# Kernel tuning notes

Hardware: AMD Instinct MI355X
Metric: run time of the kernel (lower is better)

## Reference

```python
import jax, jax.numpy as jnp
import numpy as np

EPS = 1e-5
D_MODEL, D_STATE, D_CONV, D_INNER, NHEADS, HEADDIM = 256, 64, 4, 512, 8, 64
CONV_DIM = D_INNER + 2 * D_STATE          # 640
D_IN_PROJ = 2 * D_INNER + 2 * D_STATE + NHEADS  # 1160


def _conv_bn_relu(h, w, b, g, beta, m, v, stride, pad):
    # Conv2d + eval-mode BatchNorm2d + ReLU (dropout = identity in eval)
    y = jax.lax.conv_general_dilated(h, w, stride, pad,
                                     dimension_numbers=("NCHW", "OIHW", "NCHW"))
    y = y + b[None, :, None, None]
    scale = (g / jnp.sqrt(v + EPS))[None, :, None, None]
    y = (y - m[None, :, None, None]) * scale + beta[None, :, None, None]
    return jax.nn.relu(y)


def _forward(x, c1w, c1b, bn1g, bn1b, bn1m, bn1v,
             c2w, c2b, bn2g, bn2b, bn2m, bn2v,
             c3w, c3b, bn3g, bn3b, bn3m, bn3v,
             mw_in, mconv_w, mconv_b, mdt_bias, mA_log, mD, mnorm_w, mw_out,
             f1w, f1b, bn4g, bn4b, bn4m, bn4v, f2w, f2b):
    Bsz = x.shape[0]
    h = x[:, None, :, :]                                        # (B,1,H,W)
    h = _conv_bn_relu(h, c1w, c1b, bn1g, bn1b, bn1m, bn1v, (1, 4), [(0, 0), (25, 25)])
    h = jax.lax.reduce_window(h, -jnp.inf, jax.lax.max,
                              (1, 1, 1, 4), (1, 1, 1, 4), "VALID")  # MaxPool (1,4)
    h = _conv_bn_relu(h, c2w, c2b, bn2g, bn2b, bn2m, bn2v, (1, 2), [(0, 0), (10, 10)])
    h = _conv_bn_relu(h, c3w, c3b, bn3g, bn3b, bn3m, bn3v, (1, 2), [(0, 0), (4, 4)])
    h = jnp.mean(h, axis=(2, 3))                                # AdaptiveAvgPool2d((1,1)) -> (B,256)
    xs = h[:, None, :]                                          # (B, L=1, d_model)
    L = xs.shape[1]

    # ---- Mamba2 block ----
    zxbcdt = xs @ mw_in.T                                       # (B,L,1160)
    z = zxbcdt[..., :D_INNER]
    xBC = zxbcdt[..., D_INNER:D_INNER + CONV_DIM]
    dt = zxbcdt[..., -NHEADS:]

    # causal depthwise conv1d + silu
    xc = jnp.transpose(xBC, (0, 2, 1))                          # (B,conv_dim,L)
    xc = jnp.pad(xc, ((0, 0), (0, 0), (D_CONV - 1, 0)))
    xc = jax.lax.conv_general_dilated(xc, mconv_w, (1,), [(0, 0)],
                                      feature_group_count=CONV_DIM,
                                      dimension_numbers=("NCH", "OIH", "NCH"))
    xc = xc + mconv_b[None, :, None]
    xBC = jax.nn.silu(jnp.transpose(xc, (0, 2, 1)))

    xin = xBC[..., :D_INNER]
    Bm = xBC[..., D_INNER:D_INNER + D_STATE]                    # (B,L,d_state), ngroups=1
    Cm = xBC[..., -D_STATE:]

    dt = jax.nn.softplus(dt + mdt_bias)                         # (B,L,nh)
    A = -jnp.exp(mA_log)                                        # (nh,)
    xh = xin.reshape(Bsz, L, NHEADS, HEADDIM)
    dA = jnp.exp(dt * A)                                        # (B,L,nh)
    dtx = dt[..., None] * xh                                    # (B,L,nh,hd)

    def step(hstate, t):
        dA_t, dtx_t, B_t, C_t = t
        hstate = dA_t[:, :, None, None] * hstate + dtx_t[..., None] * B_t[:, None, None, :]
        y_t = jnp.einsum("bhpn,bn->bhp", hstate, C_t)
        return hstate, y_t

    h0 = jnp.zeros((Bsz, NHEADS, HEADDIM, D_STATE), xs.dtype)
    _, ys = jax.lax.scan(step, h0, (jnp.moveaxis(dA, 1, 0), jnp.moveaxis(dtx, 1, 0),
                                    jnp.moveaxis(Bm, 1, 0), jnp.moveaxis(Cm, 1, 0)))
    y = jnp.moveaxis(ys, 0, 1) + mD[None, None, :, None] * xh   # (B,L,nh,hd)
    y = y.reshape(Bsz, L, D_INNER)

    # gated RMSNorm then out_proj
    y = y * jax.nn.silu(z)
    y = y * jax.lax.rsqrt(jnp.mean(y * y, axis=-1, keepdims=True) + EPS) * mnorm_w
    out = (y @ mw_out.T)[:, 0, :]                               # squeeze(1) -> (B,256)

    # ---- classifier: Linear + BN1d(eval) + ReLU + Linear ----
    o = out @ f1w.T + f1b
    o = (o - bn4m) * (bn4g / jnp.sqrt(bn4v + EPS)) + bn4b
    o = jax.nn.relu(o)
    o = o @ f2w.T + f2b                                         # (B,1)
    return o


def setup_inputs() -> dict:
    key = jax.random.key(0)
    ks = iter(jax.random.split(key, 48))

    def n(shape, s=0.02):
        return jax.random.normal(next(ks), shape, jnp.float32) * s

    B, H, W = 256, 2, 3840
    inp = {
        "x": jax.random.normal(next(ks), (B, H, W), jnp.float32),
        "c1w": n((64, 1, 1, 51)), "c1b": jnp.zeros(64),
        "bn1g": jnp.ones(64), "bn1b": jnp.zeros(64), "bn1m": jnp.zeros(64), "bn1v": jnp.ones(64),
        "c2w": n((128, 64, 1, 21)), "c2b": jnp.zeros(128),
        "bn2g": jnp.ones(128), "bn2b": jnp.zeros(128), "bn2m": jnp.zeros(128), "bn2v": jnp.ones(128),
        "c3w": n((256, 128, 1, 9)), "c3b": jnp.zeros(256),
        "bn3g": jnp.ones(256), "bn3b": jnp.zeros(256), "bn3m": jnp.zeros(256), "bn3v": jnp.ones(256),
        "mw_in": n((D_IN_PROJ, D_MODEL)),
        "mconv_w": n((CONV_DIM, 1, D_CONV), 0.1), "mconv_b": jnp.zeros(CONV_DIM),
        "mdt_bias": n((NHEADS,), 0.1),
        "mA_log": jnp.log(jnp.arange(1, NHEADS + 1, dtype=jnp.float32)),
        "mD": jnp.ones(NHEADS),
        "mnorm_w": jnp.ones(D_INNER),
        "mw_out": n((D_MODEL, D_INNER)),
        "f1w": n((64, 256)), "f1b": jnp.zeros(64),
        "bn4g": jnp.ones(64), "bn4b": jnp.zeros(64), "bn4m": jnp.zeros(64), "bn4v": jnp.ones(64),
        "f2w": n((1, 64)), "f2b": jnp.zeros(1),
    }
    return inp


def reference(x, c1w, c1b, bn1g, bn1b, bn1m, bn1v,
              c2w, c2b, bn2g, bn2b, bn2m, bn2v,
              c3w, c3b, bn3g, bn3b, bn3m, bn3v,
              mw_in, mconv_w, mconv_b, mdt_bias, mA_log, mD, mnorm_w, mw_out,
              f1w, f1b, bn4g, bn4b, bn4m, bn4v, f2w, f2b):
    return _forward(x, c1w, c1b, bn1g, bn1b, bn1m, bn1v,
                    c2w, c2b, bn2g, bn2b, bn2m, bn2v,
                    c3w, c3b, bn3g, bn3b, bn3m, bn3v,
                    mw_in, mconv_w, mconv_b, mdt_bias, mA_log, mD, mnorm_w, mw_out,
                    f1w, f1b, bn4g, bn4b, bn4m, bn4v, f2w, f2b)
```

## Files before the change

kernel.cpp:

```cpp
#include <hip/hip_runtime.h>
#include <math.h>

#define EPS 1e-5f

typedef _Float16 f16x8 __attribute__((ext_vector_type(8)));
typedef _Float16 f16x4 __attribute__((ext_vector_type(4)));
typedef float    f32x4 __attribute__((ext_vector_type(4)));

__device__ __forceinline__ void gload16(const void* g, void* l) {
  __builtin_amdgcn_global_load_lds(
      (const __attribute__((address_space(1))) void*)g,
      (__attribute__((address_space(3))) void*)l, 16, 0, 0);
}

__global__ void k0_prep(const float* __restrict__ c2w, const float* __restrict__ c3w,
                        const float* __restrict__ c2b, const float* __restrict__ bn2g,
                        const float* __restrict__ bn2b, const float* __restrict__ bn2m,
                        const float* __restrict__ bn2v,
                        const float* __restrict__ c3b, const float* __restrict__ bn3g,
                        const float* __restrict__ bn3b, const float* __restrict__ bn3m,
                        const float* __restrict__ bn3v,
                        const float* __restrict__ mw_in, const float* __restrict__ mw_out,
                        const float* __restrict__ f1w, const float* __restrict__ f1b,
                        const float* __restrict__ bn4g, const float* __restrict__ bn4b,
                        const float* __restrict__ bn4m, const float* __restrict__ bn4v,
                        const float* __restrict__ c1w, const float* __restrict__ c1b,
                        const float* __restrict__ bn1g, const float* __restrict__ bn1b,
                        const float* __restrict__ bn1m, const float* __restrict__ bn1v,
                        _Float16* __restrict__ wA2h, _Float16* __restrict__ wA3h,
                        _Float16* __restrict__ wInH, _Float16* __restrict__ wOutH,
                        _Float16* __restrict__ f1H, _Float16* __restrict__ wA1h,
                        float* __restrict__ scbi) {
  int idx = blockIdx.x * blockDim.x + threadIdx.x;
  int stride = gridDim.x * blockDim.x;
  for (int i = idx; i < 172032; i += stride) {
    int j = i & 7; int t = i >> 3; int co = t & 127; int sg = t >> 7;
    int kglob = sg * 8 + j;
    int ci = kglob & 63, kk = kglob >> 6;
    wA2h[i] = (_Float16)c2w[(co * 64 + ci) * 21 + kk];
  }
  for (int i = idx; i < 294912; i += stride) {
    int j = i & 7; int t = i >> 3; int co = t & 255; int sg = t >> 8;
    int kglob = sg * 8 + j;
    int ci = kglob & 127, kk = kglob >> 7;
    wA3h[i] = (_Float16)c3w[(co * 128 + ci) * 9 + kk];
  }
  for (int i = idx; i < 1216 * 256; i += stride) {
    int row = i >> 8;
    wInH[i] = (row < 1160) ? (_Float16)mw_in[i] : (_Float16)0.f;
  }
  for (int i = idx; i < 256 * 512; i += stride) wOutH[i] = (_Float16)mw_out[i];
  for (int i = idx; i < 64 * 256; i += stride)  f1H[i]  = (_Float16)f1w[i];
  for (int i = idx; i < 4096; i += stride) {
    int kglob = i & 63, co = i >> 6;
    int r = kglob >> 4, q = kglob & 15;
    int k = 4 * q + r;
    wA1h[i] = (k < 51) ? (_Float16)c1w[co * 51 + k] : (_Float16)0.f;
  }
  if (idx < 128) {
    float sc = bn2g[idx] / sqrtf(bn2v[idx] + EPS);
    scbi[idx] = sc;
    scbi[128 + idx] = (c2b[idx] - bn2m[idx]) * sc + bn2b[idx];
  }
  if (idx < 256) {
    float sc = bn3g[idx] / sqrtf(bn3v[idx] + EPS);
    scbi[256 + idx] = sc;
    scbi[512 + idx] = (c3b[idx] - bn3m[idx]) * sc + bn3b[idx];
  }
  if (idx < 64) {
    float sc = bn4g[idx] / sqrtf(bn4v[idx] + EPS);
    scbi[768 + idx] = sc;
    scbi[832 + idx] = (f1b[idx] - bn4m[idx]) * sc + bn4b[idx];
  }
  if (idx >= 64 && idx < 128) {
    int c = idx - 64;
    float sc = bn1g[c] / sqrtf(bn1v[c] + EPS);
    scbi[896 + c] = sc;
    scbi[960 + c] = (c1b[c] - bn1m[c]) * sc + bn1b[c];
  }
}

__global__ __launch_bounds__(256) void k1_conv1_pool(
    const float* __restrict__ x, const _Float16* __restrict__ wA1h,
    const float* __restrict__ scbi, _Float16* __restrict__ p1h) {
  __shared__ float phx[4 * 980];
  __shared__ __align__(16) _Float16 outs[240 * 64];
  int br = blockIdx.x, tid = threadIdx.x;
  for (int i = tid; i < 3920; i += 256) phx[i] = 0.f;
  {
    float4 z4 = make_float4(0.f, 0.f, 0.f, 0.f);
    for (int i = tid; i < 1920; i += 256) ((float4*)outs)[i] = z4;
  }
  __syncthreads();
  const float* xrow = x + (size_t)br * 3840;
  for (int i = tid; i < 960; i += 256) {
    float4 v = ((const float4*)xrow)[i];
    int g = 4 * i;
    #pragma unroll
    for (int c = 0; c < 4; ++c) {
      int gp = g + c + 25;
      phx[(gp & 3) * 980 + (gp >> 2)] = ((const float*)&v)[c];
    }
  }
  int l = tid & 63, wv = tid >> 6;
  int lr = l & 15, lg = l >> 4;
  f16x8 af[2][4];
  #pragma unroll
  for (int s = 0; s < 2; ++s)
    #pragma unroll
    for (int mm = 0; mm < 4; ++mm)
      af[s][mm] = *(const f16x8*)&wA1h[(mm * 16 + lr) * 64 + s * 32 + lg * 8];
  float scr[4][4], bir[4][4];
  #pragma unroll
  for (int mm = 0; mm < 4; ++mm)
    #pragma unroll
    for (int r2 = 0; r2 < 4; ++r2) {
      int co = mm * 16 + lg * 4 + r2;
      scr[mm][r2] = scbi[896 + co];
      bir[mm][r2] = scbi[960 + co];
    }
  __syncthreads();
  for (int it = 0; it < 15; ++it) {
    int w0 = (wv + 4 * it) * 16;
    f32x4 acc[4] = {};
    #pragma unroll
    for (int s = 0; s < 2; ++s) {
      int r = s * 2 + (lg >> 1), q0 = (lg & 1) * 8;
      const float* src = &phx[r * 980 + w0 + lr + q0];
      f16x8 bf;
      #pragma unroll
      for (int j = 0; j < 8; ++j) bf[j] = (_Float16)src[j];
      #pragma unroll
      for (int mm = 0; mm < 4; ++mm)
        acc[mm] = __builtin_amdgcn_mfma_f32_16x16x32_f16(af[s][mm], bf, acc[mm], 0, 0, 0);
    }
    int pp = (w0 >> 2) + (lr >> 2);
    #pragma unroll
    for (int mm = 0; mm < 4; ++mm) {
      int co0 = mm * 16 + lg * 4;
      f16x4 hv;
      #pragma unroll
      for (int r2 = 0; r2 < 4; ++r2) {
        float v0 = acc[mm][r2] * scr[mm][r2] + bir[mm][r2];
        float m1 = fmaxf(v0, __shfl_xor(v0, 1));
        float m2 = fmaxf(m1, __shfl_xor(m1, 2));
        hv[r2] = (_Float16)fmaxf(m2, 0.f);
      }
      if ((lr & 3) == 0)
        *(f16x4*)&outs[pp * 64 + co0] = hv;
    }
  }
  __syncthreads();
  _Float16* dst = p1h + (size_t)br * 18432;
  for (int h = tid; h < 2304; h += 256) {
    int p = h >> 3, cp = h & 7;
    float4 val = make_float4(0.f, 0.f, 0.f, 0.f);
    if (p >= 10 && p < 250) {
      int ci0 = (cp ^ ((p >> 1) & 7)) * 8;
      val = *(const float4*)&outs[(p - 10) * 64 + ci0];
    }
    *(float4*)&dst[h * 8] = val;
  }
}

__global__ __launch_bounds__(512) void k23_conv23(
    const _Float16* __restrict__ p1h, const _Float16* __restrict__ wA2h,
    const _Float16* __restrict__ wA3h, const float* __restrict__ scbi,
    float* __restrict__ part) {
  __shared__ __align__(16) _Float16 buf[18432];
  _Float16* xT  = buf;
  _Float16* h2T = buf;
  int br = blockIdx.x, tid = threadIdx.x;
  const char* xsrc = (const char*)(p1h + (size_t)br * 18432);
  for (int i = tid; i < 2304; i += 512)
    gload16(xsrc + i * 16, (char*)xT + i * 16);
  int l = tid & 63, wv = tid >> 6;
  int lr = l & 15, lg = l >> 4;
  int cobase = (wv >> 1) * 32, wbase = (wv & 1) * 64;
  int arow2 = lg * 128 + cobase + lr;
  int wn[4], wn128[4];
  #pragma unroll
  for (int nn = 0; nn < 4; ++nn) { wn[nn] = wbase + nn * 16 + lr; wn128[nn] = wn[nn] * 128; }
  f32x4 acc[2][4] = {};
  const _Float16* wa2 = wA2h + (size_t)arow2 * 8;
  f16x8 afE[2], afO[2];
  afE[0] = *(const f16x8*)&wa2[0];
  afE[1] = *(const f16x8*)&wa2[128];
  afO[0] = *(const f16x8*)&wa2[4096];
  afO[1] = *(const f16x8*)&wa2[4096 + 128];
  __syncthreads();
  #pragma unroll 1
  for (int sp = 0; sp < 21; ++sp) {
    int sp64 = sp * 64;
    int sph = sp >> 1;
    f16x8 bf0[4], bf1[4];
    #pragma unroll
    for (int nn = 0; nn < 4; ++nn) {
      int t = (wn[nn] + sph) & 7;
      int i0 = wn128[nn] + sp64 + ((lg ^ t) << 3);
      bf0[nn] = *(const f16x8*)&xT[i0];
      bf1[nn] = *(const f16x8*)&xT[i0 ^ 32];
    }
    #pragma unroll
    for (int mm = 0; mm < 2; ++mm)
      #pragma unroll
      for (int nn = 0; nn < 4; ++nn)
        acc[mm][nn] = __builtin_amdgcn_mfma_f32_16x16x32_f16(afE[mm], bf0[nn], acc[mm][nn], 0, 0, 0);
    if (sp < 20) {
      const _Float16* wsrc = wa2 + (size_t)(2 * sp + 2) * 4096;
      afE[0] = *(const f16x8*)&wsrc[0];
      afE[1] = *(const f16x8*)&wsrc[128];
    }
    #pragma unroll
    for (int mm = 0; mm < 2; ++mm)
      #pragma unroll
      for (int nn = 0; nn < 4; ++nn)
        acc[mm][nn] = __builtin_amdgcn_mfma_f32_16x16x32_f16(afO[mm], bf1[nn], acc[mm][nn], 0, 0, 0);
    if (sp < 20) {
      const _Float16* wsrc = wa2 + (size_t)(2 * sp + 3) * 4096;
      afO[0] = *(const f16x8*)&wsrc[0];
      afO[1] = *(const f16x8*)&wsrc[128];
    }
  }
  __syncthreads();
  {
    float4 z4 = make_float4(0.f, 0.f, 0.f, 0.f);
    for (int i = tid; i < 384; i += 512) {
      int h8 = (i < 64) ? i : (1984 + (i - 64));
      *(float4*)&h2T[h8 * 8] = z4;
    }
    const float* sc2 = scbi;
    const float* bi2 = scbi + 128;
    #pragma unroll
    for (int mm = 0; mm < 2; ++mm) {
      int co0 = cobase + mm * 16 + lg * 4;
      float s0 = sc2[co0], s1 = sc2[co0 + 1], s2 = sc2[co0 + 2], s3 = sc2[co0 + 3];
      float b0 = bi2[co0], b1 = bi2[co0 + 1], b2 = bi2[co0 + 2], b3 = bi2[co0 + 3];
      #pragma unroll
      for (int nn = 0; nn < 4; ++nn) {
        int w = wn[nn];
        if (w < 120) {
          int p3 = 4 + w;
          f16x4 hv;
          hv[0] = (_Float16)fmaxf(acc[mm][nn][0] * s0 + b0, 0.f);
          hv[1] = (_Float16)fmaxf(acc[mm][nn][1] * s1 + b1, 0.f);
          hv[2] = (_Float16)fmaxf(acc[mm][nn][2] * s2 + b2, 0.f);
          hv[3] = (_Float16)fmaxf(acc[mm][nn][3] * s3 + b3, 0.f);
          int cp = (co0 >> 3) ^ ((p3 >> 1) & 15);
          *(f16x4*)&h2T[p3 * 128 + cp * 8 + (co0 & 7)] = hv;
        }
      }
    }
  }
  int cobase3 = wv * 32;
  int arow3 = lg * 256 + cobase3 + lr;
  const _Float16* wa3 = wA3h + (size_t)arow3 * 8;
  int wn3[4], wn256[4];
  #pragma unroll
  for (int nn = 0; nn < 4; ++nn) { wn3[nn] = nn * 16 + lr; wn256[nn] = wn3[nn] * 256; }
  f32x4 acc3[2][4] = {};
  f16x8 ag[4][2];
  #pragma unroll
  for (int j = 0; j < 4; ++j) {
    ag[j][0] = *(const f16x8*)&wa3[(size_t)j * 8192];
    ag[j][1] = *(const f16x8*)&wa3[(size_t)j * 8192 + 128];
  }
  __syncthreads();
  #pragma unroll 1
  for (int q = 0; q < 9; ++q) {
    int q128 = q << 7;
    int qh = q >> 1;
    int i0[4];
    #pragma unroll
    for (int nn = 0; nn < 4; ++nn) {
      int t = (wn3[nn] + qh) & 15;
      i0[nn] = wn256[nn] + q128 + ((lg ^ t) << 3);
    }
    #pragma unroll
    for (int j = 0; j < 4; ++j) {
      f16x8 bg[4];
      #pragma unroll
      for (int nn = 0; nn < 4; ++nn)
        bg[nn] = *(const f16x8*)&h2T[i0[nn] ^ (j << 5)];
      #pragma unroll
      for (int mm = 0; mm < 2; ++mm)
        #pragma unroll
        for (int nn = 0; nn < 4; ++nn)
          acc3[mm][nn] = __builtin_amdgcn_mfma_f32_16x16x32_f16(ag[j][mm], bg[nn], acc3[mm][nn], 0, 0, 0);
      if (q < 8) {
        const _Float16* wsrc = wa3 + (size_t)(4 * (q + 1) + j) * 8192;
        ag[j][0] = *(const f16x8*)&wsrc[0];
        ag[j][1] = *(const f16x8*)&wsrc[128];
      }
    }
  }
  {
    const float* sc3 = scbi + 256;
    const float* bi3 = scbi + 512;
    #pragma unroll
    for (int mm = 0; mm < 2; ++mm) {
      #pragma unroll
      for (int r = 0; r < 4; ++r) {
        int co = cobase3 + mm * 16 + lg * 4 + r;
        float sc = sc3[co], bi = bi3[co];
        float sum = 0.f;
        #pragma unroll
        for (int nn = 0; nn < 4; ++nn) {
          int w = wn3[nn];
          float val = fmaxf(acc3[mm][nn][r] * sc + bi, 0.f);
          if (w < 60) sum += val;
        }
        sum += __shfl_xor(sum, 1);
        sum += __shfl_xor(sum, 2);
        sum += __shfl_xor(sum, 4);
        sum += __shfl_xor(sum, 8);
        if (lr == 0) part[(size_t)br * 256 + co] = sum;
      }
    }
  }
}

__global__ __launch_bounds__(256) void k4a_gemm_in(
    const _Float16* __restrict__ wInH, const float* __restrict__ part,
    float* __restrict__ Z) {
  __shared__ __align__(16) _Float16 featL[64][264];
  int tid = threadIdx.x;
  int mbase = blockIdx.x * 64, nbase = blockIdx.y * 64;
  for (int i = tid; i < 64 * 256; i += 256) {
    int b = i >> 8, c = i & 255;
    float s0 = part[((size_t)(nbase + b) * 2 + 0) * 256 + c];
    float s1 = part[((size_t)(nbase + b) * 2 + 1) * 256 + c];
    featL[b][c] = (_Float16)((s0 + s1) * (1.f / 120.f));
  }
  int l = tid & 63, wv = tid >> 6;
  int lr = l & 15, lg = l >> 4;
  int mo = (wv & 1) * 32, no = (wv >> 1) * 32;
  f32x4 acc[2][2] = {};
  __syncthreads();
  for (int s = 0; s < 8; ++s) {
    f16x8 af[2], bf[2];
    #pragma unroll
    for (int mm = 0; mm < 2; ++mm) {
      int row = mbase + mo + mm * 16 + lr;
      af[mm] = *(const f16x8*)&wInH[(size_t)row * 256 + s * 32 + lg * 8];
    }
    #pragma unroll
    for (int nn = 0; nn < 2; ++nn) {
      int b = no + nn * 16 + lr;
      bf[nn] = *(const f16x8*)&featL[b][s * 32 + lg * 8];
    }
    #pragma unroll
    for (int mm = 0; mm < 2; ++mm)
      #pragma unroll
      for (int nn = 0; nn < 2; ++nn)
        acc[mm][nn] = __builtin_amdgcn_mfma_f32_16x16x32_f16(af[mm], bf[nn], acc[mm][nn], 0, 0, 0);
  }
  #pragma unroll
  for (int mm = 0; mm < 2; ++mm) {
    int row0 = mbase + mo + mm * 16 + lg * 4;
    #pragma unroll
    for (int nn = 0; nn < 2; ++nn) {
      int b = nbase + no + nn * 16 + lr;
      *(float4*)&Z[(size_t)b * 1216 + row0] = *(float4*)&acc[mm][nn];
    }
  }
}

__global__ __launch_bounds__(256) void k4b_pointwise(
    const float* __restrict__ Z,
    const float* __restrict__ mconv_w, const float* __restrict__ mconv_b,
    const float* __restrict__ mdt_bias, const float* __restrict__ mD,
    const float* __restrict__ mnorm_w, _Float16* __restrict__ yH) {
  __shared__ float zx[1160];
  __shared__ float red4[4];
  __shared__ float sBs;
  __shared__ float coef[8];
  int tid = threadIdx.x;
  int b = blockIdx.x;
  const float* zsrc = Z + (size_t)b * 1216;
  for (int row = tid; row < 1160; row += 256) zx[row] = zsrc[row];
  __syncthreads();
  for (int c = tid; c < 640; c += 256) {
    float t = zx[512 + c] * mconv_w[c * 4 + 3] + mconv_b[c];
    zx[512 + c] = t / (1.f + expf(-t));
  }
  __syncthreads();
  if (tid < 64) {
    float p = zx[1024 + tid] * zx[1088 + tid];
    #pragma unroll
    for (int off = 32; off > 0; off >>= 1) p += __shfl_xor(p, off, 64);
    if (tid == 0) sBs = p;
  }
  __syncthreads();
  if (tid < 8) {
    float u = zx[1152 + tid] + mdt_bias[tid];
    float sp = (u > 20.f) ? u : log1pf(expf(u));
    coef[tid] = sp * sBs + mD[tid];
  }
  __syncthreads();
  float ssq = 0.f;
  #pragma unroll
  for (int ii = 0; ii < 2; ++ii) {
    int i = tid + ii * 256;
    float z = zx[i];
    float t = zx[512 + i] * coef[i >> 6] * (z / (1.f + expf(-z)));
    zx[i] = t;
    ssq += t * t;
  }
  #pragma unroll
  for (int off = 32; off > 0; off >>= 1) ssq += __shfl_xor(ssq, off, 64);
  if ((tid & 63) == 0) red4[tid >> 6] = ssq;
  __syncthreads();
  {
    float total = red4[0] + red4[1] + red4[2] + red4[3];
    float rn = 1.f / sqrtf(total * (1.f / 512.f) + EPS);
    #pragma unroll
    for (int ii = 0; ii < 2; ++ii) {
      int i = tid + ii * 256;
      float y = zx[i] * rn * mnorm_w[i];
      yH[(size_t)b * 512 + i] = (_Float16)y;
    }
  }
}

__global__ __launch_bounds__(256) void k4c_gemm_out(
    const _Float16* __restrict__ wOutH, const _Float16* __restrict__ yH,
    _Float16* __restrict__ obH) {
  int tid = threadIdx.x;
  int mbase = blockIdx.x * 64, nbase = blockIdx.y * 64;
  int l = tid & 63, wv = tid >> 6;
  int lr = l & 15, lg = l >> 4;
  int mo = (wv & 1) * 32, no = (wv >> 1) * 32;
  f32x4 acc[2][2] = {};
  for (int s = 0; s < 16; ++s) {
    f16x8 af[2], bf[2];
    #pragma unroll
    for (int mm = 0; mm < 2; ++mm) {
      int row = mbase + mo + mm * 16 + lr;
      af[mm] = *(const f16x8*)&wOutH[(size_t)row * 512 + s * 32 + lg * 8];
    }
    #pragma unroll
    for (int nn = 0; nn < 2; ++nn) {
      int b = nbase + no + nn * 16 + lr;
      bf[nn] = *(const f16x8*)&yH[(size_t)b * 512 + s * 32 + lg * 8];
    }
    #pragma unroll
    for (int mm = 0; mm < 2; ++mm)
      #pragma unroll
      for (int nn = 0; nn < 2; ++nn)
        acc[mm][nn] = __builtin_amdgcn_mfma_f32_16x16x32_f16(af[mm], bf[nn], acc[mm][nn], 0, 0, 0);
  }
  #pragma unroll
  for (int mm = 0; mm < 2; ++mm) {
    int row0 = mbase + mo + mm * 16 + lg * 4;
    #pragma unroll
    for (int nn = 0; nn < 2; ++nn) {
      int b = nbase + no + nn * 16 + lr;
      f16x4 hv;
      hv[0] = (_Float16)acc[mm][nn][0];
      hv[1] = (_Float16)acc[mm][nn][1];
      hv[2] = (_Float16)acc[mm][nn][2];
      hv[3] = (_Float16)acc[mm][nn][3];
      *(f16x4*)&obH[(size_t)b * 256 + row0] = hv;
    }
  }
}

__global__ __launch_bounds__(256) void k4d_head(
    const _Float16* __restrict__ f1H, const _Float16* __restrict__ obH,
    const float* __restrict__ scbi, const float* __restrict__ f2w,
    const float* __restrict__ f2b, float* __restrict__ outp) {
  int tid = threadIdx.x;
  int nbase = blockIdx.x * 64;
  int l = tid & 63, wv = tid >> 6;
  int lr = l & 15, lg = l >> 4;
  int bcol = nbase + wv * 16 + lr;
  f32x4 acc[4] = {};
  for (int s = 0; s < 8; ++s) {
    f16x8 bf = *(const f16x8*)&obH[(size_t)bcol * 256 + s * 32 + lg * 8];
    #pragma unroll
    for (int mm = 0; mm < 4; ++mm) {
      f16x8 af = *(const f16x8*)&f1H[(size_t)(mm * 16 + lr) * 256 + s * 32 + lg * 8];
      acc[mm] = __builtin_amdgcn_mfma_f32_16x16x32_f16(af, bf, acc[mm], 0, 0, 0);
    }
  }
  float psum = 0.f;
  #pragma unroll
  for (int mm = 0; mm < 4; ++mm) {
    #pragma unroll
    for (int r = 0; r < 4; ++r) {
      int row = mm * 16 + lg * 4 + r;
      float val = acc[mm][r] * scbi[768 + row] + scbi[832 + row];
      val = fmaxf(val, 0.f);
      psum += val * f2w[row];
    }
  }
  psum += __shfl_xor(psum, 16, 64);
  psum += __shfl_xor(psum, 32, 64);
  if (l < 16) outp[bcol] = psum + f2b[0];
}

extern "C" void kernel_launch(void* const* d_in, const int* in_sizes, int n_in,
                              void* d_out, int out_size, void* d_ws, size_t ws_size,
                              hipStream_t stream) {
  const float* x    = (const float*)d_in[0];
  const float* c1w  = (const float*)d_in[1];
  const float* c1b  = (const float*)d_in[2];
  const float* bn1g = (const float*)d_in[3];
  const float* bn1b = (const float*)d_in[4];
  const float* bn1m = (const float*)d_in[5];
  const float* bn1v = (const float*)d_in[6];
  const float* c2w  = (const float*)d_in[7];
  const float* c2b  = (const float*)d_in[8];
  const float* bn2g = (const float*)d_in[9];
  const float* bn2b = (const float*)d_in[10];
  const float* bn2m = (const float*)d_in[11];
  const float* bn2v = (const float*)d_in[12];
  const float* c3w  = (const float*)d_in[13];
  const float* c3b  = (const float*)d_in[14];
  const float* bn3g = (const float*)d_in[15];
  const float* bn3b = (const float*)d_in[16];
  const float* bn3m = (const float*)d_in[17];
  const float* bn3v = (const float*)d_in[18];
  const float* mw_in    = (const float*)d_in[19];
  const float* mconv_w  = (const float*)d_in[20];
  const float* mconv_b  = (const float*)d_in[21];
  const float* mdt_bias = (const float*)d_in[22];
  const float* mD       = (const float*)d_in[24];
  const float* mnorm_w  = (const float*)d_in[25];
  const float* mw_out   = (const float*)d_in[26];
  const float* f1w  = (const float*)d_in[27];
  const float* f1b  = (const float*)d_in[28];
  const float* bn4g = (const float*)d_in[29];
  const float* bn4b = (const float*)d_in[30];
  const float* bn4m = (const float*)d_in[31];
  const float* bn4v = (const float*)d_in[32];
  const float* f2w  = (const float*)d_in[33];
  const float* f2b  = (const float*)d_in[34];

  _Float16* p1h   = (_Float16*)d_ws;
  _Float16* h2h   = p1h + (size_t)512 * 18432;
  _Float16* wA2h  = h2h + (size_t)512 * 18432;
  _Float16* wA3h  = wA2h + 172032;
  _Float16* wInH  = wA3h + 294912;
  _Float16* wOutH = wInH + (size_t)1216 * 256;
  _Float16* f1H   = wOutH + (size_t)256 * 512;
  _Float16* featH = f1H + 64 * 256;
  _Float16* yH    = featH + 256 * 256;
  _Float16* obH   = yH + (size_t)256 * 512;
  _Float16* wA1h  = obH + 256 * 256;
  float*    scbi  = (float*)(wA1h + 4096);
  float*    part  = scbi + 1024;
  float*    Z     = part + (size_t)512 * 256;
  float*    outp  = (float*)d_out;

  k0_prep<<<dim3(512), dim3(256), 0, stream>>>(c2w, c3w, c2b, bn2g, bn2b, bn2m, bn2v,
                                               c3b, bn3g, bn3b, bn3m, bn3v,
                                               mw_in, mw_out, f1w, f1b, bn4g, bn4b, bn4m, bn4v,
                                               c1w, c1b, bn1g, bn1b, bn1m, bn1v,
                                               wA2h, wA3h, wInH, wOutH, f1H, wA1h, scbi);
  k1_conv1_pool<<<dim3(512), dim3(256), 0, stream>>>(x, wA1h, scbi, p1h);
  k23_conv23<<<dim3(512), dim3(512), 0, stream>>>(p1h, wA2h, wA3h, scbi, part);
  k4a_gemm_in<<<dim3(19, 4), dim3(256), 0, stream>>>(wInH, part, Z);
  k4b_pointwise<<<dim3(256), dim3(256), 0, stream>>>(Z, mconv_w, mconv_b, mdt_bias, mD, mnorm_w, yH);
  k4c_gemm_out<<<dim3(4, 4), dim3(256), 0, stream>>>(wOutH, yH, obH);
  k4d_head<<<dim3(4), dim3(256), 0, stream>>>(f1H, obH, scbi, f2w, f2b, outp);
}
```

Before: 103.1 us.

## Retile conv2/conv3 warps to 64-channel tiles with double-buffered weights and setprio

Changes the per-wave tiling in the fused conv2/conv3 kernel from 32 output channels by 64 positions to 64 channels by 32 positions. Each wave now loads more weight fragments from global memory but fewer LDS activation fragments. Conv3 weights are now double-buffered one k-step ahead instead of being held for four steps at once. MFMA bursts are wrapped in s_setprio, and launch bounds request 4 waves per SIMD. Because conv3 now splits the width across two waves, partial sums go through an LDS scratch reduction and an extra barrier.

After: 110.5 us. 1.07x slower.

```diff
diff --git a/kernel.cpp b/kernel.cpp
--- a/kernel.cpp
+++ b/kernel.cpp
@@ -163,7 +163,7 @@
   }
 }
 
-__global__ __launch_bounds__(512) void k23_conv23(
+__global__ __launch_bounds__(512, 4) void k23_conv23(
     const _Float16* __restrict__ p1h, const _Float16* __restrict__ wA2h,
     const _Float16* __restrict__ wA3h, const float* __restrict__ scbi,
     float* __restrict__ part) {
@@ -176,50 +176,55 @@
     gload16(xsrc + i * 16, (char*)xT + i * 16);
   int l = tid & 63, wv = tid >> 6;
   int lr = l & 15, lg = l >> 4;
-  int cobase = (wv >> 1) * 32, wbase = (wv & 1) * 64;
+  int cobase = (wv >> 2) * 64, wbase = (wv & 3) * 32;
   int arow2 = lg * 128 + cobase + lr;
-  int wn[4], wn128[4];
-  #pragma unroll
-  for (int nn = 0; nn < 4; ++nn) { wn[nn] = wbase + nn * 16 + lr; wn128[nn] = wn[nn] * 128; }
-  f32x4 acc[2][4] = {};
+  int wn[2], wn128[2];
+  #pragma unroll
+  for (int nn = 0; nn < 2; ++nn) { wn[nn] = wbase + nn * 16 + lr; wn128[nn] = wn[nn] * 128; }
+  f32x4 acc[4][2] = {};
   const _Float16* wa2 = wA2h + (size_t)arow2 * 8;
-  f16x8 afE[2], afO[2];
-  afE[0] = *(const f16x8*)&wa2[0];
-  afE[1] = *(const f16x8*)&wa2[128];
-  afO[0] = *(const f16x8*)&wa2[4096];
-  afO[1] = *(const f16x8*)&wa2[4096 + 128];
+  f16x8 afE[4], afO[4];
+  #pragma unroll
+  for (int mm = 0; mm < 4; ++mm) {
+    afE[mm] = *(const f16x8*)&wa2[mm * 128];
+    afO[mm] = *(const f16x8*)&wa2[4096 + mm * 128];
+  }
   __syncthreads();
   #pragma unroll 1
   for (int sp = 0; sp < 21; ++sp) {
     int sp64 = sp * 64;
     int sph = sp >> 1;
-    f16x8 bf0[4], bf1[4];
-    #pragma unroll
-    for (int nn = 0; nn < 4; ++nn) {
+    f16x8 bf0[2], bf1[2];
+    #pragma unroll
+    for (int nn = 0; nn < 2; ++nn) {
       int t = (wn[nn] + sph) & 7;
       int i0 = wn128[nn] + sp64 + ((lg ^ t) << 3);
       bf0[nn] = *(const f16x8*)&xT[i0];
       bf1[nn] = *(const f16x8*)&xT[i0 ^ 32];
     }
-    #pragma unroll
-    for (int mm = 0; mm < 2; ++mm)
-      #pragma unroll
-      for (int nn = 0; nn < 4; ++nn)
+    __builtin_amdgcn_s_setprio(1);
+    #pragma unroll
+    for (int mm = 0; mm < 4; ++mm)
+      #pragma unroll
+      for (int nn = 0; nn < 2; ++nn)
         acc[mm][nn] = __builtin_amdgcn_mfma_f32_16x16x32_f16(afE[mm], bf0[nn], acc[mm][nn], 0, 0, 0);
+    __builtin_amdgcn_s_setprio(0);
     if (sp < 20) {
       const _Float16* wsrc = wa2 + (size_t)(2 * sp + 2) * 4096;
-      afE[0] = *(const f16x8*)&wsrc[0];
-      afE[1] = *(const f16x8*)&wsrc[128];
-    }
-    #pragma unroll
-    for (int mm = 0; mm < 2; ++mm)
-      #pragma unroll
-      for (int nn = 0; nn < 4; ++nn)
+      #pragma unroll
+      for (int mm = 0; mm < 4; ++mm) afE[mm] = *(const f16x8*)&wsrc[mm * 128];
+    }
+    __builtin_amdgcn_s_setprio(1);
+    #pragma unroll
+    for (int mm = 0; mm < 4; ++mm)
+      #pragma unroll
+      for (int nn = 0; nn < 2; ++nn)
         acc[mm][nn] = __builtin_amdgcn_mfma_f32_16x16x32_f16(afO[mm], bf1[nn], acc[mm][nn], 0, 0, 0);
+    __builtin_amdgcn_s_setprio(0);
     if (sp < 20) {
       const _Float16* wsrc = wa2 + (size_t)(2 * sp + 3) * 4096;
-      afO[0] = *(const f16x8*)&wsrc[0];
-      afO[1] = *(const f16x8*)&wsrc[128];
+      #pragma unroll
+      for (int mm = 0; mm < 4; ++mm) afO[mm] = *(const f16x8*)&wsrc[mm * 128];
     }
   }
   __syncthreads();
@@ -232,12 +237,12 @@
     const float* sc2 = scbi;
     const float* bi2 = scbi + 128;
     #pragma unroll
-    for (int mm = 0; mm < 2; ++mm) {
+    for (int mm = 0; mm < 4; ++mm) {
       int co0 = cobase + mm * 16 + lg * 4;
       float s0 = sc2[co0], s1 = sc2[co0 + 1], s2 = sc2[co0 + 2], s3 = sc2[co0 + 3];
       float b0 = bi2[co0], b1 = bi2[co0 + 1], b2 = bi2[co0 + 2], b3 = bi2[co0 + 3];
       #pragma unroll
-      for (int nn = 0; nn < 4; ++nn) {
+      for (int nn = 0; nn < 2; ++nn) {
         int w = wn[nn];
         if (w < 120) {
           int p3 = 4 + w;
@@ -252,70 +257,77 @@
       }
     }
   }
-  int cobase3 = wv * 32;
+  int cobase3 = (wv >> 1) * 64, wbase3 = (wv & 1) * 32;
   int arow3 = lg * 256 + cobase3 + lr;
   const _Float16* wa3 = wA3h + (size_t)arow3 * 8;
-  int wn3[4], wn256[4];
-  #pragma unroll
-  for (int nn = 0; nn < 4; ++nn) { wn3[nn] = nn * 16 + lr; wn256[nn] = wn3[nn] * 256; }
-  f32x4 acc3[2][4] = {};
-  f16x8 ag[4][2];
-  #pragma unroll
-  for (int j = 0; j < 4; ++j) {
-    ag[j][0] = *(const f16x8*)&wa3[(size_t)j * 8192];
-    ag[j][1] = *(const f16x8*)&wa3[(size_t)j * 8192 + 128];
-  }
+  int wn3[2], wn256[2];
+  #pragma unroll
+  for (int nn = 0; nn < 2; ++nn) { wn3[nn] = wbase3 + nn * 16 + lr; wn256[nn] = wn3[nn] * 256; }
+  f32x4 acc3[4][2] = {};
+  f16x8 ag[2][4];
+  #pragma unroll
+  for (int mm = 0; mm < 4; ++mm) ag[0][mm] = *(const f16x8*)&wa3[mm * 128];
   __syncthreads();
   #pragma unroll 1
   for (int q = 0; q < 9; ++q) {
     int q128 = q << 7;
     int qh = q >> 1;
-    int i0[4];
-    #pragma unroll
-    for (int nn = 0; nn < 4; ++nn) {
+    int i0[2];
+    #pragma unroll
+    for (int nn = 0; nn < 2; ++nn) {
       int t = (wn3[nn] + qh) & 15;
       i0[nn] = wn256[nn] + q128 + ((lg ^ t) << 3);
     }
     #pragma unroll
     for (int j = 0; j < 4; ++j) {
-      f16x8 bg[4];
-      #pragma unroll
-      for (int nn = 0; nn < 4; ++nn)
+      const int cur = j & 1, nxt = cur ^ 1;
+      f16x8 bg[2];
+      #pragma unroll
+      for (int nn = 0; nn < 2; ++nn)
         bg[nn] = *(const f16x8*)&h2T[i0[nn] ^ (j << 5)];
-      #pragma unroll
-      for (int mm = 0; mm < 2; ++mm)
+      int s = 4 * q + j;
+      if (s < 35) {
+        const _Float16* wsrc = wa3 + (size_t)(s + 1) * 8192;
         #pragma unroll
-        for (int nn = 0; nn < 4; ++nn)
-          acc3[mm][nn] = __builtin_amdgcn_mfma_f32_16x16x32_f16(ag[j][mm], bg[nn], acc3[mm][nn], 0, 0, 0);
-      if (q < 8) {
-        const _Float16* wsrc = wa3 + (size_t)(4 * (q + 1) + j) * 8192;
-        ag[j][0] = *(const f16x8*)&wsrc[0];
-        ag[j][1] = *(const f16x8*)&wsrc[128];
+        for (int mm = 0; mm < 4; ++mm) ag[nxt][mm] = *(const f16x8*)&wsrc[mm * 128];
       }
-    }
-  }
+      __builtin_amdgcn_s_setprio(1);
+      #pragma unroll
+      for (int mm = 0; mm < 4; ++mm)
+        #pragma unroll
+        for (int nn = 0; nn < 2; ++nn)
+          acc3[mm][nn] = __builtin_amdgcn_mfma_f32_16x16x32_f16(ag[cur][mm], bg[nn], acc3[mm][nn], 0, 0, 0);
+      __builtin_amdgcn_s_setprio(0);
+    }
+  }
+  __syncthreads();
   {
+    float* scratch = (float*)buf;
     const float* sc3 = scbi + 256;
     const float* bi3 = scbi + 512;
     #pragma unroll
-    for (int mm = 0; mm < 2; ++mm) {
+    for (int mm = 0; mm < 4; ++mm) {
       #pragma unroll
       for (int r = 0; r < 4; ++r) {
-        int co = cobase3 + mm * 16 + lg * 4 + r;
-        float sc = sc3[co], bi = bi3[co];
+        int cidx = mm * 16 + lg * 4 + r;
+        float sc = sc3[cobase3 + cidx], bi = bi3[cobase3 + cidx];
         float sum = 0.f;
         #pragma unroll
-        for (int nn = 0; nn < 4; ++nn) {
-          int w = wn3[nn];
+        for (int nn = 0; nn < 2; ++nn) {
           float val = fmaxf(acc3[mm][nn][r] * sc + bi, 0.f);
-          if (w < 60) sum += val;
+          if (wn3[nn] < 60) sum += val;
         }
         sum += __shfl_xor(sum, 1);
         sum += __shfl_xor(sum, 2);
         sum += __shfl_xor(sum, 4);
         sum += __shfl_xor(sum, 8);
-        if (lr == 0) part[(size_t)br * 256 + co] = sum;
+        if (lr == 0) scratch[wv * 64 + cidx] = sum;
       }
+    }
+    __syncthreads();
+    if (tid < 256) {
+      int p = tid >> 6, c = tid & 63;
+      part[(size_t)br * 256 + tid] = scratch[(2 * p) * 64 + c] + scratch[(2 * p + 1) * 64 + c];
     }
   }
 }
```

## Fuse out-projection GEMM and classifier head into one kernel via LDS

Applied to the files above, without the earlier changes.

Merges the Mamba out-projection GEMM and the FC head into a single kernel. Each block computes a full 256x64 output tile and keeps it in swizzled shared memory instead of writing it to global memory, then runs the head GEMM from LDS. This removes one kernel launch and a global round trip of the intermediate. In exchange, the grid shrinks from 16 blocks to 4, and each wave does four times the MFMA work with more accumulator registers.

New measurement: 111.9 us. +8.5%, slower.

```diff
diff --git a/kernel.cpp b/kernel.cpp
--- a/kernel.cpp
+++ b/kernel.cpp
@@ -423,81 +423,82 @@
   }
 }
 
-__global__ __launch_bounds__(256) void k4c_gemm_out(
+__global__ __launch_bounds__(256) void k4cd_out_head(
     const _Float16* __restrict__ wOutH, const _Float16* __restrict__ yH,
-    _Float16* __restrict__ obH) {
-  int tid = threadIdx.x;
-  int mbase = blockIdx.x * 64, nbase = blockIdx.y * 64;
-  int l = tid & 63, wv = tid >> 6;
-  int lr = l & 15, lg = l >> 4;
-  int mo = (wv & 1) * 32, no = (wv >> 1) * 32;
-  f32x4 acc[2][2] = {};
-  for (int s = 0; s < 16; ++s) {
-    f16x8 af[2], bf[2];
-    #pragma unroll
-    for (int mm = 0; mm < 2; ++mm) {
-      int row = mbase + mo + mm * 16 + lr;
-      af[mm] = *(const f16x8*)&wOutH[(size_t)row * 512 + s * 32 + lg * 8];
-    }
-    #pragma unroll
-    for (int nn = 0; nn < 2; ++nn) {
-      int b = nbase + no + nn * 16 + lr;
-      bf[nn] = *(const f16x8*)&yH[(size_t)b * 512 + s * 32 + lg * 8];
-    }
-    #pragma unroll
-    for (int mm = 0; mm < 2; ++mm)
-      #pragma unroll
-      for (int nn = 0; nn < 2; ++nn)
-        acc[mm][nn] = __builtin_amdgcn_mfma_f32_16x16x32_f16(af[mm], bf[nn], acc[mm][nn], 0, 0, 0);
-  }
-  #pragma unroll
-  for (int mm = 0; mm < 2; ++mm) {
-    int row0 = mbase + mo + mm * 16 + lg * 4;
-    #pragma unroll
-    for (int nn = 0; nn < 2; ++nn) {
-      int b = nbase + no + nn * 16 + lr;
-      f16x4 hv;
-      hv[0] = (_Float16)acc[mm][nn][0];
-      hv[1] = (_Float16)acc[mm][nn][1];
-      hv[2] = (_Float16)acc[mm][nn][2];
-      hv[3] = (_Float16)acc[mm][nn][3];
-      *(f16x4*)&obH[(size_t)b * 256 + row0] = hv;
-    }
-  }
-}
-
-__global__ __launch_bounds__(256) void k4d_head(
-    const _Float16* __restrict__ f1H, const _Float16* __restrict__ obH,
-    const float* __restrict__ scbi, const float* __restrict__ f2w,
-    const float* __restrict__ f2b, float* __restrict__ outp) {
+    const _Float16* __restrict__ f1H, const float* __restrict__ scbi,
+    const float* __restrict__ f2w, const float* __restrict__ f2b,
+    float* __restrict__ outp) {
+  __shared__ __align__(16) _Float16 obL[64 * 264];
   int tid = threadIdx.x;
   int nbase = blockIdx.x * 64;
   int l = tid & 63, wv = tid >> 6;
   int lr = l & 15, lg = l >> 4;
-  int bcol = nbase + wv * 16 + lr;
-  f32x4 acc[4] = {};
-  for (int s = 0; s < 8; ++s) {
-    f16x8 bf = *(const f16x8*)&obH[(size_t)bcol * 256 + s * 32 + lg * 8];
+  {
+    int mbase = wv * 64;
+    f32x4 acc[4][4] = {};
+    for (int s = 0; s < 16; ++s) {
+      f16x8 af[4], bf[4];
+      #pragma unroll
+      for (int mm = 0; mm < 4; ++mm) {
+        int row = mbase + mm * 16 + lr;
+        af[mm] = *(const f16x8*)&wOutH[(size_t)row * 512 + s * 32 + lg * 8];
+      }
+      #pragma unroll
+      for (int nn = 0; nn < 4; ++nn) {
+        int b = nbase + nn * 16 + lr;
+        bf[nn] = *(const f16x8*)&yH[(size_t)b * 512 + s * 32 + lg * 8];
+      }
+      #pragma unroll
+      for (int mm = 0; mm < 4; ++mm)
+        #pragma unroll
+        for (int nn = 0; nn < 4; ++nn)
+          acc[mm][nn] = __builtin_amdgcn_mfma_f32_16x16x32_f16(af[mm], bf[nn], acc[mm][nn], 0, 0, 0);
+    }
     #pragma unroll
     for (int mm = 0; mm < 4; ++mm) {
-      f16x8 af = *(const f16x8*)&f1H[(size_t)(mm * 16 + lr) * 256 + s * 32 + lg * 8];
-      acc[mm] = __builtin_amdgcn_mfma_f32_16x16x32_f16(af, bf, acc[mm], 0, 0, 0);
-    }
-  }
-  float psum = 0.f;
-  #pragma unroll
-  for (int mm = 0; mm < 4; ++mm) {
-    #pragma unroll
-    for (int r = 0; r < 4; ++r) {
-      int row = mm * 16 + lg * 4 + r;
-      float val = acc[mm][r] * scbi[768 + row] + scbi[832 + row];
-      val = fmaxf(val, 0.f);
-      psum += val * f2w[row];
-    }
-  }
-  psum += __shfl_xor(psum, 16, 64);
-  psum += __shfl_xor(psum, 32, 64);
-  if (l < 16) outp[bcol] = psum + f2b[0];
+      int row0 = mbase + mm * 16 + lg * 4;
+      int cw = row0 >> 3, half = (row0 >> 2) & 1;
+      #pragma unroll
+      for (int nn = 0; nn < 4; ++nn) {
+        int b = nn * 16 + lr;
+        f16x4 hv;
+        hv[0] = (_Float16)acc[mm][nn][0];
+        hv[1] = (_Float16)acc[mm][nn][1];
+        hv[2] = (_Float16)acc[mm][nn][2];
+        hv[3] = (_Float16)acc[mm][nn][3];
+        *(f16x4*)&obL[b * 264 + (cw ^ (b & 7)) * 8 + half * 4] = hv;
+      }
+    }
+  }
+  __syncthreads();
+  {
+    int bloc = wv * 16 + lr;
+    int bcol = nbase + bloc;
+    f32x4 acc2[4] = {};
+    for (int s = 0; s < 8; ++s) {
+      int c = s * 4 + lg;
+      f16x8 bf = *(const f16x8*)&obL[bloc * 264 + (c ^ (bloc & 7)) * 8];
+      #pragma unroll
+      for (int mm = 0; mm < 4; ++mm) {
+        f16x8 af = *(const f16x8*)&f1H[(size_t)(mm * 16 + lr) * 256 + s * 32 + lg * 8];
+        acc2[mm] = __builtin_amdgcn_mfma_f32_16x16x32_f16(af, bf, acc2[mm], 0, 0, 0);
+      }
+    }
+    float psum = 0.f;
+    #pragma unroll
+    for (int mm = 0; mm < 4; ++mm) {
+      #pragma unroll
+      for (int r = 0; r < 4; ++r) {
+        int row = mm * 16 + lg * 4 + r;
+        float val = acc2[mm][r] * scbi[768 + row] + scbi[832 + row];
+        val = fmaxf(val, 0.f);
+        psum += val * f2w[row];
+      }
+    }
+    psum += __shfl_xor(psum, 16, 64);
+    psum += __shfl_xor(psum, 32, 64);
+    if (l < 16) outp[bcol] = psum + f2b[0];
+  }
 }
 
 extern "C" void kernel_launch(void* const* d_in, const int* in_sizes, int n_in,
@@ -563,6 +564,5 @@
   k23_conv23<<<dim3(512), dim3(512), 0, stream>>>(p1h, wA2h, wA3h, scbi, part);
   k4a_gemm_in<<<dim3(19, 4), dim3(256), 0, stream>>>(wInH, part, Z);
   k4b_pointwise<<<dim3(256), dim3(256), 0, stream>>>(Z, mconv_w, mconv_b, mdt_bias, mD, mnorm_w, yH);
-  k4c_gemm_out<<<dim3(4, 4), dim3(256), 0, stream>>>(wOutH, yH, obH);
-  k4d_head<<<dim3(4), dim3(256), 0, stream>>>(f1H, obH, scbi, f2w, f2b, outp);
-}
+  k4cd_out_head<<<dim3(4), dim3(256), 0, stream>>>(wOutH, yH, f1H, scbi, f2w, f2b, outp);
+}
```

## Fuse conv1+maxpool into conv2/conv3 kernel, keeping pooled activations in LDS

Applied to the files above, without the earlier changes.

Merges the conv1+BN+ReLU+maxpool kernel into the conv2/conv3 kernel. The pooled fp16 activations are written straight into the swizzled LDS buffer that conv2 reads, so the global round trip through p1h and one kernel launch go away. The fused kernel runs 512 threads with a launch-bounds occupancy hint, and LDS use per block grows because phx and buf now coexist. That may lower occupancy or change register pressure.

Result: faster. 88.59 us (-14.1%).

```diff
diff --git a/kernel.cpp b/kernel.cpp
--- a/kernel.cpp
+++ b/kernel.cpp
@@ -6,12 +6,6 @@
 typedef _Float16 f16x8 __attribute__((ext_vector_type(8)));
 typedef _Float16 f16x4 __attribute__((ext_vector_type(4)));
 typedef float    f32x4 __attribute__((ext_vector_type(4)));
-
-__device__ __forceinline__ void gload16(const void* g, void* l) {
-  __builtin_amdgcn_global_load_lds(
-      (const __attribute__((address_space(1))) void*)g,
-      (__attribute__((address_space(3))) void*)l, 16, 0, 0);
-}
 
 __global__ void k0_prep(const float* __restrict__ c2w, const float* __restrict__ c3w,
                         const float* __restrict__ c2b, const float* __restrict__ bn2g,
@@ -80,102 +74,87 @@
   }
 }
 
-__global__ __launch_bounds__(256) void k1_conv1_pool(
+__global__ __launch_bounds__(512, 4) void k123_conv123(
     const float* __restrict__ x, const _Float16* __restrict__ wA1h,
-    const float* __restrict__ scbi, _Float16* __restrict__ p1h) {
+    const _Float16* __restrict__ wA2h, const _Float16* __restrict__ wA3h,
+    const float* __restrict__ scbi, float* __restrict__ part) {
   __shared__ float phx[4 * 980];
-  __shared__ __align__(16) _Float16 outs[240 * 64];
-  int br = blockIdx.x, tid = threadIdx.x;
-  for (int i = tid; i < 3920; i += 256) phx[i] = 0.f;
-  {
-    float4 z4 = make_float4(0.f, 0.f, 0.f, 0.f);
-    for (int i = tid; i < 1920; i += 256) ((float4*)outs)[i] = z4;
-  }
-  __syncthreads();
-  const float* xrow = x + (size_t)br * 3840;
-  for (int i = tid; i < 960; i += 256) {
-    float4 v = ((const float4*)xrow)[i];
-    int g = 4 * i;
-    #pragma unroll
-    for (int c = 0; c < 4; ++c) {
-      int gp = g + c + 25;
-      phx[(gp & 3) * 980 + (gp >> 2)] = ((const float*)&v)[c];
-    }
-  }
-  int l = tid & 63, wv = tid >> 6;
-  int lr = l & 15, lg = l >> 4;
-  f16x8 af[2][4];
-  #pragma unroll
-  for (int s = 0; s < 2; ++s)
-    #pragma unroll
-    for (int mm = 0; mm < 4; ++mm)
-      af[s][mm] = *(const f16x8*)&wA1h[(mm * 16 + lr) * 64 + s * 32 + lg * 8];
-  float scr[4][4], bir[4][4];
-  #pragma unroll
-  for (int mm = 0; mm < 4; ++mm)
-    #pragma unroll
-    for (int r2 = 0; r2 < 4; ++r2) {
-      int co = mm * 16 + lg * 4 + r2;
-      scr[mm][r2] = scbi[896 + co];
-      bir[mm][r2] = scbi[960 + co];
-    }
-  __syncthreads();
-  for (int it = 0; it < 15; ++it) {
-    int w0 = (wv + 4 * it) * 16;
-    f32x4 acc[4] = {};
-    #pragma unroll
-    for (int s = 0; s < 2; ++s) {
-      int r = s * 2 + (lg >> 1), q0 = (lg & 1) * 8;
-      const float* src = &phx[r * 980 + w0 + lr + q0];
-      f16x8 bf;
-      #pragma unroll
-      for (int j = 0; j < 8; ++j) bf[j] = (_Float16)src[j];
-      #pragma unroll
-      for (int mm = 0; mm < 4; ++mm)
-        acc[mm] = __builtin_amdgcn_mfma_f32_16x16x32_f16(af[s][mm], bf, acc[mm], 0, 0, 0);
-    }
-    int pp = (w0 >> 2) + (lr >> 2);
-    #pragma unroll
-    for (int mm = 0; mm < 4; ++mm) {
-      int co0 = mm * 16 + lg * 4;
-      f16x4 hv;
-      #pragma unroll
-      for (int r2 = 0; r2 < 4; ++r2) {
-        float v0 = acc[mm][r2] * scr[mm][r2] + bir[mm][r2];
-        float m1 = fmaxf(v0, __shfl_xor(v0, 1));
-        float m2 = fmaxf(m1, __shfl_xor(m1, 2));
-        hv[r2] = (_Float16)fmaxf(m2, 0.f);
-      }
-      if ((lr & 3) == 0)
-        *(f16x4*)&outs[pp * 64 + co0] = hv;
-    }
-  }
-  __syncthreads();
-  _Float16* dst = p1h + (size_t)br * 18432;
-  for (int h = tid; h < 2304; h += 256) {
-    int p = h >> 3, cp = h & 7;
-    float4 val = make_float4(0.f, 0.f, 0.f, 0.f);
-    if (p >= 10 && p < 250) {
-      int ci0 = (cp ^ ((p >> 1) & 7)) * 8;
-      val = *(const float4*)&outs[(p - 10) * 64 + ci0];
-    }
-    *(float4*)&dst[h * 8] = val;
-  }
-}
-
-__global__ __launch_bounds__(512) void k23_conv23(
-    const _Float16* __restrict__ p1h, const _Float16* __restrict__ wA2h,
-    const _Float16* __restrict__ wA3h, const float* __restrict__ scbi,
-    float* __restrict__ part) {
   __shared__ __align__(16) _Float16 buf[18432];
   _Float16* xT  = buf;
   _Float16* h2T = buf;
   int br = blockIdx.x, tid = threadIdx.x;
-  const char* xsrc = (const char*)(p1h + (size_t)br * 18432);
-  for (int i = tid; i < 2304; i += 512)
-    gload16(xsrc + i * 16, (char*)xT + i * 16);
+  for (int i = tid; i < 3920; i += 512) phx[i] = 0.f;
+  {
+    float4 z4 = make_float4(0.f, 0.f, 0.f, 0.f);
+    for (int i = tid; i < 80; i += 512)  ((float4*)xT)[i] = z4;
+    for (int i = tid; i < 304; i += 512) ((float4*)(xT + 16000))[i] = z4;
+  }
+  __syncthreads();
+  const float* xrow = x + (size_t)br * 3840;
+  for (int i = tid; i < 960; i += 512) {
+    float4 v = ((const float4*)xrow)[i];
+    int g = 4 * i;
+    #pragma unroll
+    for (int c = 0; c < 4; ++c) {
+      int gp = g + c + 25;
+      phx[(gp & 3) * 980 + (gp >> 2)] = ((const float*)&v)[c];
+    }
+  }
   int l = tid & 63, wv = tid >> 6;
   int lr = l & 15, lg = l >> 4;
+  {
+    f16x8 af1[2][4];
+    #pragma unroll
+    for (int s = 0; s < 2; ++s)
+      #pragma unroll
+      for (int mm = 0; mm < 4; ++mm)
+        af1[s][mm] = *(const f16x8*)&wA1h[(mm * 16 + lr) * 64 + s * 32 + lg * 8];
+    float scr[4][4], bir[4][4];
+    #pragma unroll
+    for (int mm = 0; mm < 4; ++mm)
+      #pragma unroll
+      for (int r2 = 0; r2 < 4; ++r2) {
+        int co = mm * 16 + lg * 4 + r2;
+        scr[mm][r2] = scbi[896 + co];
+        bir[mm][r2] = scbi[960 + co];
+      }
+    __syncthreads();
+    for (int it = 0; it < 8; ++it) {
+      int g = wv + 8 * it;
+      if (g < 60) {
+        int w0 = g * 16;
+        f32x4 acc1[4] = {};
+        #pragma unroll
+        for (int s = 0; s < 2; ++s) {
+          int r = s * 2 + (lg >> 1), q0 = (lg & 1) * 8;
+          const float* src = &phx[r * 980 + w0 + lr + q0];
+          f16x8 bf;
+          #pragma unroll
+          for (int j = 0; j < 8; ++j) bf[j] = (_Float16)src[j];
+          #pragma unroll
+          for (int mm = 0; mm < 4; ++mm)
+            acc1[mm] = __builtin_amdgcn_mfma_f32_16x16x32_f16(af1[s][mm], bf, acc1[mm], 0, 0, 0);
+        }
+        int pp = w0 / 4 + (lr >> 2);
+        int p = pp + 10;
+        int cpx = (p >> 1) & 7;
+        #pragma unroll
+        for (int mm = 0; mm < 4; ++mm) {
+          int co0 = mm * 16 + lg * 4;
+          f16x4 hv;
+          #pragma unroll
+          for (int r2 = 0; r2 < 4; ++r2) {
+            float v0 = acc1[mm][r2] * scr[mm][r2] + bir[mm][r2];
+            float m1 = fmaxf(v0, __shfl_xor(v0, 1));
+            float m2 = fmaxf(m1, __shfl_xor(m1, 2));
+            hv[r2] = (_Float16)fmaxf(m2, 0.f);
+          }
+          if ((lr & 3) == 0)
+            *(f16x4*)&xT[p * 64 + ((co0 >> 3) ^ cpx) * 8 + (co0 & 7)] = hv;
+        }
+      }
+    }
+  }
   int cobase = (wv >> 1) * 32, wbase = (wv & 1) * 64;
   int arow2 = lg * 128 + cobase + lr;
   int wn[4], wn128[4];
@@ -559,8 +538,7 @@
                                                mw_in, mw_out, f1w, f1b, bn4g, bn4b, bn4m, bn4v,
                                                c1w, c1b, bn1g, bn1b, bn1m, bn1v,
                                                wA2h, wA3h, wInH, wOutH, f1H, wA1h, scbi);
-  k1_conv1_pool<<<dim3(512), dim3(256), 0, stream>>>(x, wA1h, scbi, p1h);
-  k23_conv23<<<dim3(512), dim3(512), 0, stream>>>(p1h, wA2h, wA3h, scbi, part);
+  k123_conv123<<<dim3(512), dim3(512), 0, stream>>>(x, wA1h, wA2h, wA3h, scbi, part);
   k4a_gemm_in<<<dim3(19, 4), dim3(256), 0, stream>>>(wInH, part, Z);
   k4b_pointwise<<<dim3(256), dim3(256), 0, stream>>>(Z, mconv_w, mconv_b, mdt_bias, mD, mnorm_w, yH);
   k4c_gemm_out<<<dim3(4, 4), dim3(256), 0, stream>>>(wOutH, yH, obH);
```
